# Performance work log

Measured on AMD Instinct MI355X. Metric: run time of the kernel, lower is better.

## Reference

```python
import jax, jax.numpy as jnp
import numpy as np

B, T, C, HS = 8, 2048, 1024, 64


def setup_inputs() -> dict:
    key = jax.random.key(0)
    ks = jax.random.split(key, 4)
    x = jax.random.normal(ks[0], (B, T, C), dtype=jnp.float32)
    Wq = jax.random.normal(ks[1], (C, HS), dtype=jnp.float32) * (C ** -0.5)
    Wk = jax.random.normal(ks[2], (C, HS), dtype=jnp.float32) * (C ** -0.5)
    Wv = jax.random.normal(ks[3], (C, HS), dtype=jnp.float32) * (C ** -0.5)
    mask = jnp.tril(jnp.ones((T, T), dtype=jnp.int32))  # causal mask
    return {"x": x, "mask": mask, "Wq": Wq, "Wk": Wk, "Wv": Wv}


def reference(x, mask, Wq, Wk, Wv):
    # x: [B,T,C]; bias-free projections to head_size
    q = jnp.einsum("btc,ch->bth", x, Wq)
    k = jnp.einsum("btc,ch->bth", x, Wk)
    v = jnp.einsum("btc,ch->bth", x, Wv)
    # NOTE: original scales by C**-0.5 (n_embd), not head_size**-0.5
    wei = jnp.einsum("bth,bsh->bts", q, k) * (x.shape[-1] ** -0.5)
    wei = jnp.where(mask[None, :, :] == 0, -jnp.inf, wei)
    wei = jax.nn.softmax(wei, axis=-1)
    # dropout is identity in eval / p=0
    out = jnp.einsum("bts,bsh->bth", wei, v)
    return out
```

## Files before the change

### kernel.cpp

```cpp
#include <hip/hip_runtime.h>
#include <hip/hip_bf16.h>


#define B_  8
#define T_  2048
#define C_  1024
#define HS_ 64
#define MROWS (B_ * T_)

typedef __attribute__((ext_vector_type(8))) short bf16x8;
typedef __attribute__((ext_vector_type(4))) float f32x4;
typedef __attribute__((ext_vector_type(4))) float float4v;

#define SCALE_LOG2 0.04508422037445829f

#define PSTR 72

__device__ __forceinline__ short f2bs(float f) {
    __hip_bfloat16 h = __float2bfloat16(f);
    short s;
    __builtin_memcpy(&s, &h, 2);
    return s;
}

__global__ __launch_bounds__(256) void wt_kernel(
    const float* __restrict__ Wq,
    const float* __restrict__ Wk,
    const float* __restrict__ Wv,
    __hip_bfloat16* __restrict__ Wt) {
    __shared__ float tile[64][65];
    const int m  = blockIdx.x >> 4;
    const int r0 = (blockIdx.x & 15) * 64;
    const float* W = (m == 0) ? Wq : (m == 1) ? Wk : Wv;
    const int i = threadIdx.x >> 6;
    const int j = threadIdx.x & 63;
#pragma unroll
    for (int p = 0; p < 16; ++p) {
        int r = p * 4 + i;
        tile[r][j] = W[(size_t)(r0 + r) * HS_ + j];
    }
    __syncthreads();
#pragma unroll
    for (int p = 0; p < 16; ++p) {
        int h = p * 4 + i;
        Wt[(size_t)m * (HS_ * C_) + (size_t)h * C_ + r0 + j] =
            __float2bfloat16(tile[j][h]);
    }
}

__global__ __launch_bounds__(256, 4) void proj_kernel(
    const float* __restrict__ x,
    const __hip_bfloat16* __restrict__ Wt,
    __hip_bfloat16* __restrict__ Q,
    __hip_bfloat16* __restrict__ Kp,
    __hip_bfloat16* __restrict__ Vt)
{
    __shared__ float xt0[32 * 68];
    __shared__ float xt1[32 * 68];

    const int lane = threadIdx.x & 63;
    const int wave = threadIdx.x >> 6;
    const int quad = lane >> 4;
    const int l15  = lane & 15;
    const int row0 = blockIdx.x * 32;

    const float* gsrc[8];
#pragma unroll
    for (int rr = 0; rr < 8; ++rr)
        gsrc[rr] = x + (size_t)(row0 + wave * 8 + rr) * C_ + lane;

    const __hip_bfloat16* wbase[3];
#pragma unroll
    for (int j = 0; j < 3; ++j) {
        int nt = wave * 3 + j;
        int h  = ((nt & 3) * 16) + l15;
        wbase[j] = Wt + (size_t)(nt >> 2) * (HS_ * C_) + (size_t)h * C_ + quad * 8;
    }

    f32x4 acc[2][3];
#pragma unroll
    for (int rt = 0; rt < 2; ++rt)
#pragma unroll
        for (int j = 0; j < 3; ++j)
            acc[rt][j] = (f32x4){0.f, 0.f, 0.f, 0.f};

    bf16x8 bfr0[2][3], bfr1[2][3];

#define ISSUE_DMA(XT, kc)                                                    \
    do {                                                                     \
        _Pragma("unroll")                                                    \
        for (int rr = 0; rr < 8; ++rr)                                       \
            __builtin_amdgcn_global_load_lds(                                \
                (const __attribute__((address_space(1))) unsigned*)          \
                    (gsrc[rr] + (kc)),                                       \
                (__attribute__((address_space(3))) unsigned*)                \
                    (&XT[(wave * 8 + rr) * 68]),                             \
                4, 0, 0);                                                    \
    } while (0)

#define LOAD_B(BF, kc)                                                       \
    do {                                                                     \
        _Pragma("unroll")                                                    \
        for (int ks = 0; ks < 2; ++ks)                                       \
            _Pragma("unroll")                                                \
            for (int j = 0; j < 3; ++j)                                      \
                BF[ks][j] = *(const bf16x8*)(wbase[j] + (kc) + ks * 32);     \
    } while (0)

#define COMPUTE(XT, BF)                                                      \
    do {                                                                     \
        _Pragma("unroll")                                                    \
        for (int ks = 0; ks < 2; ++ks) {                                     \
            bf16x8 a[2];                                                     \
            _Pragma("unroll")                                                \
            for (int rt = 0; rt < 2; ++rt) {                                 \
                const float4v* p = (const float4v*)                          \
                    &XT[(rt * 16 + l15) * 68 + ks * 32 + quad * 8];          \
                float4v f0 = p[0], f1 = p[1];                                \
                _Pragma("unroll")                                            \
                for (int e = 0; e < 4; ++e) {                                \
                    a[rt][e]     = f2bs(f0[e]);                              \
                    a[rt][4 + e] = f2bs(f1[e]);                              \
                }                                                            \
            }                                                                \
            _Pragma("unroll")                                                \
            for (int rt = 0; rt < 2; ++rt)                                   \
                _Pragma("unroll")                                            \
                for (int j = 0; j < 3; ++j)                                  \
                    acc[rt][j] = __builtin_amdgcn_mfma_f32_16x16x32_bf16(    \
                        a[rt], BF[ks][j], acc[rt][j], 0, 0, 0);              \
        }                                                                    \
    } while (0)

    ISSUE_DMA(xt0, 0);
    LOAD_B(bfr0, 0);

#pragma unroll 1
    for (int kc = 0; kc < C_; kc += 128) {
        __syncthreads();
        if (kc + 64 < C_) {
            ISSUE_DMA(xt1, kc + 64);
            LOAD_B(bfr1, kc + 64);
        }
        COMPUTE(xt0, bfr0);
        __syncthreads();
        if (kc + 128 < C_) {
            ISSUE_DMA(xt0, kc + 128);
            LOAD_B(bfr0, kc + 128);
        }
        COMPUTE(xt1, bfr1);
    }
#undef ISSUE_DMA
#undef LOAD_B
#undef COMPUTE

#pragma unroll
    for (int rt = 0; rt < 2; ++rt) {
#pragma unroll
        for (int j = 0; j < 3; ++j) {
            int nt  = wave * 3 + j;
            int mtx = nt >> 2;
            int col = (nt & 3) * 16 + l15;
#pragma unroll
            for (int r = 0; r < 4; ++r) {
                int row = row0 + rt * 16 + quad * 4 + r;
                __hip_bfloat16 v = __float2bfloat16(acc[rt][j][r]);
                if (mtx == 0) {
                    Q[(size_t)row * HS_ + col] = v;
                } else if (mtx == 1) {
                    Kp[(size_t)row * HS_ + col] = v;
                } else {
                    int bidx = row >> 11;
                    int t    = row & 2047;
                    Vt[((size_t)bidx * HS_ + col) * T_ + t] = v;
                }
            }
        }
    }
}

__global__ __launch_bounds__(256, 3) void attn_kernel(
    const __hip_bfloat16* __restrict__ Q,
    const __hip_bfloat16* __restrict__ Kp,
    const __hip_bfloat16* __restrict__ Vt,
    float* __restrict__ out)
{
    __shared__ __align__(16) char smem[4 * 32 * PSTR * 2 + 4 * 32 * 4];
    __hip_bfloat16* plds = (__hip_bfloat16*)smem;
    float* o_red = (float*)smem;
    float* l_red = (float*)(smem + 4 * 32 * PSTR * 2);

    const int tid  = threadIdx.x;
    const int wv   = tid >> 6;
    const int lane = tid & 63;
    const int quad = lane >> 4;
    const int l15  = lane & 15;
    const int b    = blockIdx.x & 7;
    const int lt   = 63 - (blockIdx.x >> 3);
    const int qb   = lt * 32;
    const int rowg = b * T_ + qb;

    __hip_bfloat16* pb = plds + wv * (32 * PSTR);

    bf16x8 qf[2][2];
#pragma unroll
    for (int rt = 0; rt < 2; ++rt)
#pragma unroll
        for (int h = 0; h < 2; ++h)
            qf[rt][h] = *(const bf16x8*)
                (Q + (size_t)(rowg + rt * 16 + l15) * HS_ + h * 32 + quad * 8);

    f32x4 o[2][4];
#pragma unroll
    for (int rt = 0; rt < 2; ++rt)
#pragma unroll
        for (int j = 0; j < 4; ++j) o[rt][j] = (f32x4){0.f, 0.f, 0.f, 0.f};
    float lp[2][4] = {{0.f,0.f,0.f,0.f},{0.f,0.f,0.f,0.f}};

    const int nt = (qb + 31) / 64 + 1;

#pragma unroll 1
    for (int t = wv; t < nt; t += 4) {
        const int kb = t * 64;
        const __hip_bfloat16* Kb = Kp + (size_t)(b * T_ + kb) * HS_;

        bf16x8 kf[4][2];
#pragma unroll
        for (int c = 0; c < 4; ++c)
#pragma unroll
            for (int h = 0; h < 2; ++h)
                kf[c][h] = *(const bf16x8*)
                    (Kb + (size_t)(c * 16 + l15) * HS_ + h * 32 + quad * 8);
        bf16x8 vf[2][4];
#pragma unroll
        for (int h = 0; h < 2; ++h)
#pragma unroll
            for (int j = 0; j < 4; ++j)
                vf[h][j] = *(const bf16x8*)
                    (Vt + ((size_t)b * HS_ + j * 16 + l15) * T_ +
                     kb + h * 32 + quad * 8);

        f32x4 s[2][4];
#pragma unroll
        for (int rt = 0; rt < 2; ++rt)
#pragma unroll
            for (int c = 0; c < 4; ++c) {
                s[rt][c] = (f32x4){0.f, 0.f, 0.f, 0.f};
                s[rt][c] = __builtin_amdgcn_mfma_f32_16x16x32_bf16(
                    qf[rt][0], kf[c][0], s[rt][c], 0, 0, 0);
                s[rt][c] = __builtin_amdgcn_mfma_f32_16x16x32_bf16(
                    qf[rt][1], kf[c][1], s[rt][c], 0, 0, 0);
            }

        const bool msk = (kb + 63 > qb);
#pragma unroll
        for (int rt = 0; rt < 2; ++rt)
#pragma unroll
            for (int c = 0; c < 4; ++c)
#pragma unroll
                for (int r = 0; r < 4; ++r) {
                    float pv = exp2f(s[rt][c][r] * SCALE_LOG2);
                    if (msk) {
                        int row = qb + rt * 16 + quad * 4 + r;
                        if (kb + c * 16 + l15 > row) pv = 0.f;
                    }
                    lp[rt][r] += pv;
                    pb[(rt * 16 + quad * 4 + r) * PSTR + c * 16 + l15] =
                        __float2bfloat16(pv);
                }
        asm volatile("s_waitcnt lgkmcnt(0)" ::: "memory");
#pragma unroll
        for (int rt = 0; rt < 2; ++rt) {
            bf16x8 pf0 = *(const bf16x8*)
                (pb + (rt * 16 + l15) * PSTR + quad * 8);
            bf16x8 pf1 = *(const bf16x8*)
                (pb + (rt * 16 + l15) * PSTR + 32 + quad * 8);
#pragma unroll
            for (int j = 0; j < 4; ++j) {
                o[rt][j] = __builtin_amdgcn_mfma_f32_16x16x32_bf16(
                    pf0, vf[0][j], o[rt][j], 0, 0, 0);
                o[rt][j] = __builtin_amdgcn_mfma_f32_16x16x32_bf16(
                    pf1, vf[1][j], o[rt][j], 0, 0, 0);
            }
        }
    }

#pragma unroll
    for (int rt = 0; rt < 2; ++rt)
#pragma unroll
        for (int r = 0; r < 4; ++r) {
            float v = lp[rt][r];
            v += __shfl_xor(v, 1);
            v += __shfl_xor(v, 2);
            v += __shfl_xor(v, 4);
            v += __shfl_xor(v, 8);
            if (l15 == 0)
                l_red[wv * 32 + rt * 16 + quad * 4 + r] = v;
        }
    __syncthreads();

    const int h  = tid & 63;
    const int rg = tid >> 6;

#pragma unroll
    for (int j = 0; j < 4; ++j)
#pragma unroll
        for (int r = 0; r < 4; ++r)
            o_red[(wv * 16 + quad * 4 + r) * 64 + j * 16 + l15] = o[0][j][r];
    __syncthreads();
#pragma unroll
    for (int k = 0; k < 4; ++k) {
        int row = rg * 4 + k;
        float s = o_red[(0 * 16 + row) * 64 + h] + o_red[(1 * 16 + row) * 64 + h]
                + o_red[(2 * 16 + row) * 64 + h] + o_red[(3 * 16 + row) * 64 + h];
        float l = l_red[row] + l_red[32 + row] + l_red[64 + row] + l_red[96 + row];
        out[(size_t)(rowg + row) * HS_ + h] = s / l;
    }
    __syncthreads();

#pragma unroll
    for (int j = 0; j < 4; ++j)
#pragma unroll
        for (int r = 0; r < 4; ++r)
            o_red[(wv * 16 + quad * 4 + r) * 64 + j * 16 + l15] = o[1][j][r];
    __syncthreads();
#pragma unroll
    for (int k = 0; k < 4; ++k) {
        int row16 = rg * 4 + k;
        int row   = 16 + row16;
        float s = o_red[(0 * 16 + row16) * 64 + h] + o_red[(1 * 16 + row16) * 64 + h]
                + o_red[(2 * 16 + row16) * 64 + h] + o_red[(3 * 16 + row16) * 64 + h];
        float l = l_red[row] + l_red[32 + row] + l_red[64 + row] + l_red[96 + row];
        out[(size_t)(rowg + row) * HS_ + h] = s / l;
    }
}

extern "C" void kernel_launch(void* const* d_in, const int* in_sizes, int n_in,
                              void* d_out, int out_size, void* d_ws, size_t ws_size,
                              hipStream_t stream) {
    (void)in_sizes; (void)n_in; (void)out_size; (void)ws_size;
    const float* x  = (const float*)d_in[0];
    const float* Wq = (const float*)d_in[2];
    const float* Wk = (const float*)d_in[3];
    const float* Wv = (const float*)d_in[4];

    __hip_bfloat16* ws = (__hip_bfloat16*)d_ws;
    __hip_bfloat16* Wt = ws;
    __hip_bfloat16* Q  = ws + 196608;
    __hip_bfloat16* Kp = ws + 196608 + 1048576;
    __hip_bfloat16* Vt = ws + 196608 + 2 * 1048576;

    wt_kernel<<<48, 256, 0, stream>>>(Wq, Wk, Wv, Wt);
    proj_kernel<<<MROWS / 32, 256, 0, stream>>>(x, Wt, Q, Kp, Vt);
    attn_kernel<<<(T_ / 32) * B_, 256, 0, stream>>>(Q, Kp, Vt, (float*)d_out);
}
```

Baseline: 156.0 us.

## Use 16-byte LDS DMA in projection and 8-wave attention blocks

The projection kernel now loads x tiles with 16-byte global_load_lds operations and a matching LDS layout with stride 260, replacing eight 4-byte DMAs per wave. The attention kernel doubles to 8 waves per block, so key blocks are split across more waves. It also interleaves K loads with score MFMAs and loads V only after the P tile is written, to cut register pressure. The final cross-wave reduction now sums 8 partials, and on early query tiles more waves may sit idle.

```diff
diff --git a/kernel.cpp b/kernel.cpp
--- a/kernel.cpp
+++ b/kernel.cpp
@@ -15,6 +15,7 @@
 #define SCALE_LOG2 0.04508422037445829f
 
 #define PSTR 72
+#define GSTR 260
 
 __device__ __forceinline__ short f2bs(float f) {
     __hip_bfloat16 h = __float2bfloat16(f);
@@ -55,8 +56,8 @@
     __hip_bfloat16* __restrict__ Kp,
     __hip_bfloat16* __restrict__ Vt)
 {
-    __shared__ float xt0[32 * 68];
-    __shared__ float xt1[32 * 68];
+    __shared__ float xt0[8 * GSTR];
+    __shared__ float xt1[8 * GSTR];
 
     const int lane = threadIdx.x & 63;
     const int wave = threadIdx.x >> 6;
@@ -64,10 +65,11 @@
     const int l15  = lane & 15;
     const int row0 = blockIdx.x * 32;
 
-    const float* gsrc[8];
-#pragma unroll
-    for (int rr = 0; rr < 8; ++rr)
-        gsrc[rr] = x + (size_t)(row0 + wave * 8 + rr) * C_ + lane;
+    const float* gsrc16[2];
+#pragma unroll
+    for (int i = 0; i < 2; ++i)
+        gsrc16[i] = x + (size_t)(row0 + wave * 8 + i * 4 + (lane >> 4)) * C_
+                      + (lane & 15) * 4;
 
     const __hip_bfloat16* wbase[3];
 #pragma unroll
@@ -89,13 +91,13 @@
 #define ISSUE_DMA(XT, kc)                                                    \
     do {                                                                     \
         _Pragma("unroll")                                                    \
-        for (int rr = 0; rr < 8; ++rr)                                       \
+        for (int i = 0; i < 2; ++i)                                          \
             __builtin_amdgcn_global_load_lds(                                \
                 (const __attribute__((address_space(1))) unsigned*)          \
-                    (gsrc[rr] + (kc)),                                       \
+                    (gsrc16[i] + (kc)),                                      \
                 (__attribute__((address_space(3))) unsigned*)                \
-                    (&XT[(wave * 8 + rr) * 68]),                             \
-                4, 0, 0);                                                    \
+                    (&XT[(wave * 2 + i) * GSTR]),                            \
+                16, 0, 0);                                                   \
     } while (0)
 
 #define LOAD_B(BF, kc)                                                       \
@@ -115,7 +117,8 @@
             _Pragma("unroll")                                                \
             for (int rt = 0; rt < 2; ++rt) {                                 \
                 const float4v* p = (const float4v*)                          \
-                    &XT[(rt * 16 + l15) * 68 + ks * 32 + quad * 8];          \
+                    &XT[(rt * 4 + (l15 >> 2)) * GSTR + (l15 & 3) * 64 +      \
+                        ks * 32 + quad * 8];                                 \
                 float4v f0 = p[0], f1 = p[1];                                \
                 _Pragma("unroll")                                            \
                 for (int e = 0; e < 4; ++e) {                                \
@@ -179,16 +182,16 @@
     }
 }
 
-__global__ __launch_bounds__(256, 3) void attn_kernel(
+__global__ __launch_bounds__(512, 4) void attn_kernel(
     const __hip_bfloat16* __restrict__ Q,
     const __hip_bfloat16* __restrict__ Kp,
     const __hip_bfloat16* __restrict__ Vt,
     float* __restrict__ out)
 {
-    __shared__ __align__(16) char smem[4 * 32 * PSTR * 2 + 4 * 32 * 4];
+    __shared__ __align__(16) char smem[8 * 32 * PSTR * 2 + 8 * 32 * 4];
     __hip_bfloat16* plds = (__hip_bfloat16*)smem;
     float* o_red = (float*)smem;
-    float* l_red = (float*)(smem + 4 * 32 * PSTR * 2);
+    float* l_red = (float*)(smem + 8 * 32 * PSTR * 2);
 
     const int tid  = threadIdx.x;
     const int wv   = tid >> 6;
@@ -220,46 +223,25 @@
     const int nt = (qb + 31) / 64 + 1;
 
 #pragma unroll 1
-    for (int t = wv; t < nt; t += 4) {
+    for (int t = wv; t < nt; t += 8) {
         const int kb = t * 64;
         const __hip_bfloat16* Kb = Kp + (size_t)(b * T_ + kb) * HS_;
-
-        bf16x8 kf[4][2];
-#pragma unroll
-        for (int c = 0; c < 4; ++c)
-#pragma unroll
-            for (int h = 0; h < 2; ++h)
-                kf[c][h] = *(const bf16x8*)
-                    (Kb + (size_t)(c * 16 + l15) * HS_ + h * 32 + quad * 8);
-        bf16x8 vf[2][4];
-#pragma unroll
-        for (int h = 0; h < 2; ++h)
-#pragma unroll
-            for (int j = 0; j < 4; ++j)
-                vf[h][j] = *(const bf16x8*)
-                    (Vt + ((size_t)b * HS_ + j * 16 + l15) * T_ +
-                     kb + h * 32 + quad * 8);
-
-        f32x4 s[2][4];
-#pragma unroll
-        for (int rt = 0; rt < 2; ++rt)
-#pragma unroll
-            for (int c = 0; c < 4; ++c) {
-                s[rt][c] = (f32x4){0.f, 0.f, 0.f, 0.f};
-                s[rt][c] = __builtin_amdgcn_mfma_f32_16x16x32_bf16(
-                    qf[rt][0], kf[c][0], s[rt][c], 0, 0, 0);
-                s[rt][c] = __builtin_amdgcn_mfma_f32_16x16x32_bf16(
-                    qf[rt][1], kf[c][1], s[rt][c], 0, 0, 0);
-            }
-
         const bool msk = (kb + 63 > qb);
-#pragma unroll
-        for (int rt = 0; rt < 2; ++rt)
-#pragma unroll
-            for (int c = 0; c < 4; ++c)
+
+#pragma unroll
+        for (int c = 0; c < 4; ++c) {
+            bf16x8 k0 = *(const bf16x8*)
+                (Kb + (size_t)(c * 16 + l15) * HS_ + quad * 8);
+            bf16x8 k1 = *(const bf16x8*)
+                (Kb + (size_t)(c * 16 + l15) * HS_ + 32 + quad * 8);
+#pragma unroll
+            for (int rt = 0; rt < 2; ++rt) {
+                f32x4 s = (f32x4){0.f, 0.f, 0.f, 0.f};
+                s = __builtin_amdgcn_mfma_f32_16x16x32_bf16(qf[rt][0], k0, s, 0, 0, 0);
+                s = __builtin_amdgcn_mfma_f32_16x16x32_bf16(qf[rt][1], k1, s, 0, 0, 0);
 #pragma unroll
                 for (int r = 0; r < 4; ++r) {
-                    float pv = exp2f(s[rt][c][r] * SCALE_LOG2);
+                    float pv = exp2f(s[r] * SCALE_LOG2);
                     if (msk) {
                         int row = qb + rt * 16 + quad * 4 + r;
                         if (kb + c * 16 + l15 > row) pv = 0.f;
@@ -268,7 +250,18 @@
                     pb[(rt * 16 + quad * 4 + r) * PSTR + c * 16 + l15] =
                         __float2bfloat16(pv);
                 }
+            }
+        }
         asm volatile("s_waitcnt lgkmcnt(0)" ::: "memory");
+
+        bf16x8 vf[2][4];
+#pragma unroll
+        for (int h = 0; h < 2; ++h)
+#pragma unroll
+            for (int j = 0; j < 4; ++j)
+                vf[h][j] = *(const bf16x8*)
+                    (Vt + ((size_t)b * HS_ + j * 16 + l15) * T_ +
+                     kb + h * 32 + quad * 8);
 #pragma unroll
         for (int rt = 0; rt < 2; ++rt) {
             bf16x8 pf0 = *(const bf16x8*)
@@ -309,11 +302,14 @@
             o_red[(wv * 16 + quad * 4 + r) * 64 + j * 16 + l15] = o[0][j][r];
     __syncthreads();
 #pragma unroll
-    for (int k = 0; k < 4; ++k) {
-        int row = rg * 4 + k;
-        float s = o_red[(0 * 16 + row) * 64 + h] + o_red[(1 * 16 + row) * 64 + h]
-                + o_red[(2 * 16 + row) * 64 + h] + o_red[(3 * 16 + row) * 64 + h];
-        float l = l_red[row] + l_red[32 + row] + l_red[64 + row] + l_red[96 + row];
+    for (int k = 0; k < 2; ++k) {
+        int row = rg * 2 + k;
+        float s = 0.f, l = 0.f;
+#pragma unroll
+        for (int w = 0; w < 8; ++w) {
+            s += o_red[(w * 16 + row) * 64 + h];
+            l += l_red[w * 32 + row];
+        }
         out[(size_t)(rowg + row) * HS_ + h] = s / l;
     }
     __syncthreads();
@@ -325,12 +321,15 @@
             o_red[(wv * 16 + quad * 4 + r) * 64 + j * 16 + l15] = o[1][j][r];
     __syncthreads();
 #pragma unroll
-    for (int k = 0; k < 4; ++k) {
-        int row16 = rg * 4 + k;
+    for (int k = 0; k < 2; ++k) {
+        int row16 = rg * 2 + k;
         int row   = 16 + row16;
-        float s = o_red[(0 * 16 + row16) * 64 + h] + o_red[(1 * 16 + row16) * 64 + h]
-                + o_red[(2 * 16 + row16) * 64 + h] + o_red[(3 * 16 + row16) * 64 + h];
-        float l = l_red[row] + l_red[32 + row] + l_red[64 + row] + l_red[96 + row];
+        float s = 0.f, l = 0.f;
+#pragma unroll
+        for (int w = 0; w < 8; ++w) {
+            s += o_red[(w * 16 + row16) * 64 + h];
+            l += l_red[w * 32 + row];
+        }
         out[(size_t)(rowg + row) * HS_ + h] = s / l;
     }
 }
@@ -352,5 +351,5 @@
 
     wt_kernel<<<48, 256, 0, stream>>>(Wq, Wk, Wv, Wt);
     proj_kernel<<<MROWS / 32, 256, 0, stream>>>(x, Wt, Q, Kp, Vt);
-    attn_kernel<<<(T_ / 32) * B_, 256, 0, stream>>>(Q, Kp, Vt, (float*)d_out);
-}
+    attn_kernel<<<(T_ / 32) * B_, 512, 0, stream>>>(Q, Kp, Vt, (float*)d_out);
+}
```

Result: slower. 161.4 us (+3.5%).
